# Optimization experiments

Measured on AMD Instinct MI355X. Metric: run time of the kernel, lower is better.

The kernel has to match this reference:

```python
import jax, jax.numpy as jnp
import numpy as np

B, HW, ENC, E, D, A, V, L = 64, 14, 2048, 512, 512, 512, 32000, 32
LN_EPS = 1e-5


def setup_inputs() -> dict:
    key = jax.random.key(0)
    ks = jax.random.split(key, 16)
    s = 0.02
    n = lambda k, sh: jax.random.normal(k, sh, jnp.float32)
    encoder_out = n(ks[0], (B, HW, HW, ENC))
    encoded_captions = jax.random.randint(ks[1], (B, L), 0, V)
    caption_lengths = jax.random.randint(ks[2], (B, 1), 2, L + 1)
    caption_lengths = caption_lengths.at[0, 0].set(L)  # ensure max length present
    return dict(
        encoder_out=encoder_out,
        encoded_captions=encoded_captions,
        caption_lengths=caption_lengths,
        emb=n(ks[3], (V, E)) * s,
        W_enc_att=n(ks[4], (A, ENC)) * s, b_enc_att=jnp.zeros((A,)),
        W_dec_att=n(ks[5], (A, D)) * s, b_dec_att=jnp.zeros((A,)),
        W_full_att=n(ks[6], (1, A)) * s, b_full_att=jnp.zeros((1,)),
        W_ih=n(ks[7], (4 * D, E + ENC)) * s, b_ih=jnp.zeros((4 * D,)),
        W_hh=n(ks[8], (4 * D, D)) * s, b_hh=jnp.zeros((4 * D,)),
        g_h=jnp.ones((D,)), be_h=jnp.zeros((D,)),
        g_c=jnp.ones((D,)), be_c=jnp.zeros((D,)),
        W_init_h=n(ks[9], (D, ENC)) * s, b_init_h=jnp.zeros((D,)),
        W_init_c=n(ks[10], (D, ENC)) * s, b_init_c=jnp.zeros((D,)),
        W_beta=n(ks[11], (ENC, D)) * s, b_beta=jnp.zeros((ENC,)),
        W_fc=n(ks[12], (V, D)) * s, b_fc=jnp.zeros((V,)),
    )


def _layer_norm(x, g, b):
    m = x.mean(-1, keepdims=True)
    v = ((x - m) ** 2).mean(-1, keepdims=True)
    return (x - m) / jnp.sqrt(v + LN_EPS) * g + b


def reference(encoder_out, encoded_captions, caption_lengths, emb,
              W_enc_att, b_enc_att, W_dec_att, b_dec_att, W_full_att, b_full_att,
              W_ih, b_ih, W_hh, b_hh, g_h, be_h, g_c, be_c,
              W_init_h, b_init_h, W_init_c, b_init_c, W_beta, b_beta, W_fc, b_fc):
    bsz = encoder_out.shape[0]
    enc_out = encoder_out.reshape(bsz, -1, encoder_out.shape[-1])  # [B,P,ENC]
    lengths = caption_lengths[:, 0]
    order = jnp.argsort(-lengths)  # stable descending sort (matches torch sort)
    lengths = lengths[order]
    enc_out = enc_out[order]
    caps = encoded_captions[order]
    embeds = emb[caps]  # [B,L,E]
    decode_lengths = lengths - 1
    T = caps.shape[1] - 1  # static max(decode_lengths)

    mean_enc = enc_out.mean(axis=1)
    h = _layer_norm(mean_enc @ W_init_h.T + b_init_h, g_h, be_h)
    c = _layer_norm(mean_enc @ W_init_c.T + b_init_c, g_c, be_c)

    att1 = enc_out @ W_enc_att.T + b_enc_att  # [B,P,A] precomputed once
    prev_seq = jnp.swapaxes(embeds[:, :T], 0, 1)  # [T,B,E] teacher-forced inputs
    masks = jnp.arange(T)[:, None] < decode_lengths[None, :]  # [T,B] active rows

    def step(carry, xs):
        h, c = carry
        prev, mask = xs
        # attention
        att2 = h @ W_dec_att.T + b_dec_att  # [B,A]
        e = jax.nn.relu(att1 + att2[:, None, :]) @ W_full_att[0] + b_full_att[0]  # [B,P]
        alpha = jax.nn.softmax(e, axis=1)
        awe = jnp.einsum('bpe,bp->be', enc_out, alpha)  # [B,ENC]
        gate = jax.nn.sigmoid(h @ W_beta.T + b_beta)
        awe = gate * awe
        # LSTM cell
        x = jnp.concatenate([prev, awe], axis=1)  # [B,E+ENC]
        gates = x @ W_ih.T + b_ih + h @ W_hh.T + b_hh
        i, f, g, o = jnp.split(gates, 4, axis=1)
        c_new = jax.nn.sigmoid(f) * c + jax.nn.sigmoid(i) * jnp.tanh(g)
        h_new = jax.nn.sigmoid(o) * jnp.tanh(c_new)
        h_new = _layer_norm(h_new, g_h, be_h)
        c_new = _layer_norm(c_new, g_c, be_c)
        preds = h_new @ W_fc.T + b_fc  # [B,V]; dropout is identity in eval
        m = mask[:, None]
        h = jnp.where(m, h_new, h)  # freeze finished rows (== torch batch shrink)
        c = jnp.where(m, c_new, c)
        return (h, c), (jnp.where(m, preds, 0.0), jnp.where(m, alpha, 0.0))

    (_, _), (preds_t, alphas_t) = jax.lax.scan(step, (h, c), (prev_seq, masks))
    predictions = jnp.swapaxes(preds_t, 0, 1)  # [B,T,V]
    alphas = jnp.swapaxes(alphas_t, 0, 1)      # [B,T,P]
    return predictions, caps, decode_lengths, alphas, order
```

## Files before the change

### kernel.cpp

```cpp
#include <hip/hip_runtime.h>
#include <cfloat>
#include <math.h>

#define B_ 64
#define P_ 196
#define ENC_ 2048
#define D_ 512
#define V_ 32000
#define L_ 32
#define T_ 31

#define OUT_PREDS 0L
#define OUT_CAPS  63488000L
#define OUT_DECL  63490048L
#define OUT_ALPH  63490112L
#define OUT_ORDER 63878976L

typedef __bf16 bf16;
typedef __bf16 bf16x8 __attribute__((ext_vector_type(8)));
typedef __bf16 bf16x4 __attribute__((ext_vector_type(4)));
typedef __bf16 bf16x2 __attribute__((ext_vector_type(2)));
typedef float  f32x4  __attribute__((ext_vector_type(4)));

static __device__ __forceinline__ float sigmoidf_(float x) { return 1.f / (1.f + __expf(-x)); }

__global__ void k_order(const int* __restrict__ cap_len, const int* __restrict__ caps,
                        int* __restrict__ order_i, int* __restrict__ declen_i,
                        int* __restrict__ caps_i, float* __restrict__ out)
{
    __shared__ int len_s[B_];
    int tid = threadIdx.x;
    len_s[tid] = cap_len[tid];
    __syncthreads();
    int li = len_s[tid];
    int pos = 0;
    for (int j = 0; j < B_; ++j) {
        int lj = len_s[j];
        pos += (lj > li) || (lj == li && j < tid);
    }
    order_i[pos]  = tid;
    declen_i[pos] = li - 1;
    out[OUT_ORDER + pos] = (float)tid;
    out[OUT_DECL  + pos] = (float)(li - 1);
    for (int l = 0; l < L_; ++l) {
        int tok = caps[tid * L_ + l];
        caps_i[pos * L_ + l] = tok;
        out[OUT_CAPS + pos * L_ + l] = (float)tok;
    }
}

__global__ __launch_bounds__(256) void k_cvt(const float* __restrict__ in, bf16* __restrict__ ob, long n)
{
    long i = ((long)blockIdx.x * 256 + threadIdx.x) * 8;
    if (i >= n) return;
    float4 a = *(const float4*)(in + i);
    float4 b = *(const float4*)(in + i + 4);
    bf16x8 v;
    v[0]=(bf16)a.x; v[1]=(bf16)a.y; v[2]=(bf16)a.z; v[3]=(bf16)a.w;
    v[4]=(bf16)b.x; v[5]=(bf16)b.y; v[6]=(bf16)b.z; v[7]=(bf16)b.w;
    *(bf16x8*)(ob + i) = v;
}

__global__ __launch_bounds__(256) void k_cvt_enc(const float* __restrict__ enc,
                                                 const int* __restrict__ order_i,
                                                 bf16* __restrict__ enc_s)
{
    long i = ((long)blockIdx.x * 256 + threadIdx.x) * 8;
    int b = (int)(i / ((long)P_ * ENC_));
    long rem = i - (long)b * P_ * ENC_;
    const float* src = enc + (long)order_i[b] * P_ * ENC_ + rem;
    float4 a = *(const float4*)(src);
    float4 c = *(const float4*)(src + 4);
    bf16x8 v;
    v[0]=(bf16)a.x; v[1]=(bf16)a.y; v[2]=(bf16)a.z; v[3]=(bf16)a.w;
    v[4]=(bf16)c.x; v[5]=(bf16)c.y; v[6]=(bf16)c.z; v[7]=(bf16)c.w;
    *(bf16x8*)(enc_s + i) = v;
}

__global__ __launch_bounds__(256) void k_meanb(const bf16* __restrict__ enc_s, bf16* __restrict__ mean_b)
{
    int b = blockIdx.x, col = blockIdx.y * 256 + threadIdx.x;
    float s = 0.f;
    const bf16* eb = enc_s + (long)b * P_ * ENC_ + col;
    for (int p = 0; p < P_; ++p) s += (float)eb[(long)p * ENC_];
    mean_b[(long)b * ENC_ + col] = (bf16)(s * (1.f / (float)P_));
}

template<int FUSE, int EPI, int SWZ>
__global__ void __launch_bounds__(256)
k_mgemm(const bf16* __restrict__ A, long lda,
        const bf16* __restrict__ B1, const bf16* __restrict__ B2,
        const float* __restrict__ bias,
        float* __restrict__ Cf, bf16* __restrict__ Cb,
        int N, int K, int kspl, int Nsp, int Ksp,
        const int* __restrict__ declen_i)
{
    const int tid = threadIdx.x;
    const int lane = tid & 63, w = tid >> 6;
    int mt, nt, z;
    if (SWZ == 0)      { mt = blockIdx.x; nt = blockIdx.y; z = blockIdx.z; }
    else if (SWZ == 1) { int o = blockIdx.x; int wg = (o & 7) * 98 + (o >> 3);
                         mt = wg >> 2; nt = wg & 3; z = 0; }
    else               { int o = blockIdx.x; int xcd = o & 7;
                         int base = xcd < 6 ? xcd * 969 : 5814 + (xcd - 6) * 968;
                         int wg = base + (o >> 3);
                         nt = wg / 31; mt = wg - 31 * nt; z = 0; }
    const int krange = K / kspl;
    const int k0 = z * krange, k1 = k0 + krange;
    const int r16 = lane & 15, kq = lane >> 4;
    const int koff = kq * 8;

    const bf16* Ap = A + (long)(mt * 64 + r16) * lda + koff;
    const int ncol0 = nt * 128 + w * 32;

    const bf16* Bp[2];
    const bf16* B2p[2];
#pragma unroll
    for (int ni = 0; ni < 2; ++ni) {
        int n = ncol0 + ni * 16 + r16;
        if (FUSE == 1)
            Bp[ni] = (n < Nsp) ? B1 + (long)n * K + koff
                               : B2 + (long)(n - Nsp) * K + koff;
        else if (FUSE == 2) {
            Bp[ni]  = B1 + (long)n * Ksp + koff;
            B2p[ni] = B2 + (long)n * (K - Ksp) + koff - Ksp;
        } else
            Bp[ni] = B1 + (long)n * K + koff;
    }

    auto loadA = [&](int kk, bf16x8* dst) {
#pragma unroll
        for (int mi = 0; mi < 4; ++mi)
            dst[mi] = *(const bf16x8*)(Ap + (long)mi * 16 * lda + kk);
    };
    auto loadB = [&](int kk, bf16x8* dst) {
#pragma unroll
        for (int ni = 0; ni < 2; ++ni) {
            if (FUSE == 2 && kk >= Ksp) dst[ni] = *(const bf16x8*)(B2p[ni] + kk);
            else                        dst[ni] = *(const bf16x8*)(Bp[ni] + kk);
        }
    };

    f32x4 acc[4][2] = {};
    bf16x8 af[4], bfr[2];
    loadA(k0, af); loadB(k0, bfr);
    for (int kk = k0 + 32; kk < k1; kk += 32) {
        bf16x8 af2[4], bf2[2];
        loadA(kk, af2); loadB(kk, bf2);
#pragma unroll
        for (int mi = 0; mi < 4; ++mi)
#pragma unroll
            for (int ni = 0; ni < 2; ++ni)
                acc[mi][ni] = __builtin_amdgcn_mfma_f32_16x16x32_bf16(bfr[ni], af[mi], acc[mi][ni], 0, 0, 0);
#pragma unroll
        for (int mi = 0; mi < 4; ++mi) af[mi] = af2[mi];
#pragma unroll
        for (int ni = 0; ni < 2; ++ni) bfr[ni] = bf2[ni];
    }
#pragma unroll
    for (int mi = 0; mi < 4; ++mi)
#pragma unroll
        for (int ni = 0; ni < 2; ++ni)
            acc[mi][ni] = __builtin_amdgcn_mfma_f32_16x16x32_bf16(bfr[ni], af[mi], acc[mi][ni], 0, 0, 0);

#pragma unroll
    for (int mi = 0; mi < 4; ++mi) {
        const int row = mt * 64 + mi * 16 + r16;
#pragma unroll
        for (int ni = 0; ni < 2; ++ni) {
            const int col = ncol0 + ni * 16 + kq * 4;
            f32x4 v = acc[mi][ni];
            if (EPI == 0) {
                *(f32x4*)(Cf + (long)z * 64 * N + (long)row * N + col) = v;
            } else if (EPI == 1) {
                f32x4 bv = *(const f32x4*)(bias + col);
                bf16x4 o;
                o[0]=(bf16)(v[0]+bv[0]); o[1]=(bf16)(v[1]+bv[1]);
                o[2]=(bf16)(v[2]+bv[2]); o[3]=(bf16)(v[3]+bv[3]);
                *(bf16x4*)(Cb + (long)row * N + col) = o;
            } else {
                int tt = row >> 6, b = row & 63;
                bool msk = tt < declen_i[b];
                f32x4 bv = *(const f32x4*)(bias + col);
                f32x4 o;
                o[0] = msk ? v[0]+bv[0] : 0.f; o[1] = msk ? v[1]+bv[1] : 0.f;
                o[2] = msk ? v[2]+bv[2] : 0.f; o[3] = msk ? v[3]+bv[3] : 0.f;
                *(f32x4*)(Cf + OUT_PREDS + ((long)b * T_ + tt) * V_ + col) = o;
            }
        }
    }
}

static __device__ __forceinline__ void ln_stats(float x, float* r1, float* r2,
                                                float& m, float& var)
{
    int tid = threadIdx.x;
    r1[tid] = x; r2[tid] = x * x;
    __syncthreads();
    for (int s = 256; s > 0; s >>= 1) {
        if (tid < s) { r1[tid] += r1[tid + s]; r2[tid] += r2[tid + s]; }
        __syncthreads();
    }
    m = r1[0] * (1.f / 512.f);
    var = r2[0] * (1.f / 512.f) - m * m;
    __syncthreads();
}

__global__ __launch_bounds__(512)
void k_initln(const float* __restrict__ pi,
              const float* __restrict__ b_h, const float* __restrict__ b_c,
              const float* __restrict__ g_h, const float* __restrict__ be_h,
              const float* __restrict__ g_c, const float* __restrict__ be_c,
              bf16* __restrict__ xh, float* __restrict__ c)
{
    int b = blockIdx.x, d = threadIdx.x;
    float yh = pi[(long)b * 1024 + d]       + b_h[d];
    float yc = pi[(long)b * 1024 + 512 + d] + b_c[d];
    __shared__ float r1[512], r2[512];
    float m, v;
    ln_stats(yh, r1, r2, m, v);
    xh[(long)b * 3072 + 2560 + d] = (bf16)((yh - m) * rsqrtf(v + 1e-5f) * g_h[d] + be_h[d]);
    ln_stats(yc, r1, r2, m, v);
    c[(long)b * 512 + d] = (yc - m) * rsqrtf(v + 1e-5f) * g_c[d] + be_c[d];
}

__global__ __launch_bounds__(256)
void k_alpha(const float* __restrict__ att2gate, const float* __restrict__ b_dec,
             const float* __restrict__ Wfull, const bf16* __restrict__ att1_b,
             const int* __restrict__ caps_i, const int* __restrict__ declen_i,
             const float* __restrict__ emb, float* __restrict__ alpha_b,
             bf16* __restrict__ xh, float* __restrict__ out, int t)
{
    const int b = blockIdx.x, tid = threadIdx.x;
    if (t >= declen_i[b]) {
        if (tid < P_) out[OUT_ALPH + ((long)b * T_ + t) * P_ + tid] = 0.f;
        return;
    }
    __shared__ float att2s[512], wf[512], red[256];
    for (int i = tid; i < 512; i += 256) {
        float s = b_dec[i];
#pragma unroll
        for (int zz = 0; zz < 4; ++zz) s += att2gate[((long)zz * 64 + b) * 2560 + i];
        att2s[i] = s;
        wf[i] = Wfull[i];
    }
    __syncthreads();
    float ev = -FLT_MAX;
    if (tid < P_) {
        const bf16* ar = att1_b + ((long)b * P_ + tid) * 512;
        float acc = 0.f;
        for (int a0 = 0; a0 < 512; a0 += 8) {
            bf16x8 v = *(const bf16x8*)(ar + a0);
#pragma unroll
            for (int j = 0; j < 8; ++j)
                acc += fmaxf((float)v[j] + att2s[a0 + j], 0.f) * wf[a0 + j];
        }
        ev = acc;
    }
    red[tid] = ev;
    __syncthreads();
    for (int s = 128; s > 0; s >>= 1) { if (tid < s) red[tid] = fmaxf(red[tid], red[tid + s]); __syncthreads(); }
    float mx = red[0];
    __syncthreads();
    float ex = (tid < P_) ? __expf(ev - mx) : 0.f;
    red[tid] = ex;
    __syncthreads();
    for (int s = 128; s > 0; s >>= 1) { if (tid < s) red[tid] += red[tid + s]; __syncthreads(); }
    float inv = 1.f / red[0];
    if (tid < P_) {
        float al = ex * inv;
        alpha_b[b * P_ + tid] = al;
        out[OUT_ALPH + ((long)b * T_ + t) * P_ + tid] = al;
    }
    int tok = caps_i[b * L_ + t];
    for (int i = tid; i < 512; i += 256)
        xh[(long)b * 3072 + i] = (bf16)emb[(long)tok * 512 + i];
}

__global__ __launch_bounds__(256)
void k_awe(const float* __restrict__ alpha_b, const float* __restrict__ att2gate,
           const float* __restrict__ b_beta, const bf16* __restrict__ enc_s,
           const int* __restrict__ declen_i, bf16* __restrict__ xh, int t)
{
    const int b = blockIdx.x, tid = threadIdx.x;
    if (t >= declen_i[b]) return;
    __shared__ float alp[P_];
    if (tid < P_) alp[tid] = alpha_b[b * P_ + tid];
    __syncthreads();
    const int col = blockIdx.y * 512 + tid * 2;
    const bf16* eb = enc_s + (long)b * P_ * ENC_ + col;
    float a0 = 0.f, a1 = 0.f;
#pragma unroll 4
    for (int p = 0; p < P_; ++p) {
        bf16x2 v = *(const bf16x2*)(eb + (long)p * ENC_);
        float al = alp[p];
        a0 += al * (float)v[0]; a1 += al * (float)v[1];
    }
    float g0 = b_beta[col], g1 = b_beta[col + 1];
#pragma unroll
    for (int zz = 0; zz < 4; ++zz) {
        const float* gs = att2gate + ((long)zz * 64 + b) * 2560 + 512 + col;
        g0 += gs[0]; g1 += gs[1];
    }
    bf16x2 o;
    o[0] = (bf16)(a0 * sigmoidf_(g0));
    o[1] = (bf16)(a1 * sigmoidf_(g1));
    *(bf16x2*)(xh + (long)b * 3072 + 512 + col) = o;
}

__global__ __launch_bounds__(512)
void k_lstm(const float* __restrict__ gp, const float* __restrict__ b_ih, const float* __restrict__ b_hh,
            const float* __restrict__ g_h, const float* __restrict__ be_h,
            const float* __restrict__ g_c, const float* __restrict__ be_c,
            bf16* __restrict__ xh, float* __restrict__ c, bf16* __restrict__ hseq,
            const int* __restrict__ declen_i, int t)
{
    int b = blockIdx.x, d = threadIdx.x;
    if (t >= declen_i[b]) return;
    float iv = b_ih[d]        + b_hh[d];
    float fv = b_ih[512 + d]  + b_hh[512 + d];
    float gv = b_ih[1024 + d] + b_hh[1024 + d];
    float ov = b_ih[1536 + d] + b_hh[1536 + d];
    for (int s = 0; s < 8; ++s) {
        const float* gs = gp + ((long)s * B_ + b) * 2048;
        iv += gs[d]; fv += gs[512 + d]; gv += gs[1024 + d]; ov += gs[1536 + d];
    }
    float cn = sigmoidf_(fv) * c[(long)b * 512 + d] + sigmoidf_(iv) * tanhf(gv);
    float hn = sigmoidf_(ov) * tanhf(cn);
    __shared__ float r1[512], r2[512];
    float m, v;
    ln_stats(hn, r1, r2, m, v);
    float hln = (hn - m) * rsqrtf(v + 1e-5f) * g_h[d] + be_h[d];
    ln_stats(cn, r1, r2, m, v);
    float cln = (cn - m) * rsqrtf(v + 1e-5f) * g_c[d] + be_c[d];
    bf16 hv = (bf16)hln;
    xh[(long)b * 3072 + 2560 + d] = hv;
    hseq[((long)t * B_ + b) * 512 + d] = hv;
    c[(long)b * 512 + d] = cln;
}

extern "C" void kernel_launch(void* const* d_in, const int* in_sizes, int n_in,
                              void* d_out, int out_size, void* d_ws, size_t ws_size,
                              hipStream_t stream)
{
    const float* enc       = (const float*)d_in[0];
    const int*   caps      = (const int*)  d_in[1];
    const int*   caplen    = (const int*)  d_in[2];
    const float* emb       = (const float*)d_in[3];
    const float* W_enc_att = (const float*)d_in[4];
    const float* b_enc_att = (const float*)d_in[5];
    const float* W_dec_att = (const float*)d_in[6];
    const float* b_dec_att = (const float*)d_in[7];
    const float* W_full    = (const float*)d_in[8];
    const float* W_ih      = (const float*)d_in[10];
    const float* b_ih      = (const float*)d_in[11];
    const float* W_hh      = (const float*)d_in[12];
    const float* b_hh      = (const float*)d_in[13];
    const float* g_h       = (const float*)d_in[14];
    const float* be_h      = (const float*)d_in[15];
    const float* g_c       = (const float*)d_in[16];
    const float* be_c      = (const float*)d_in[17];
    const float* W_init_h  = (const float*)d_in[18];
    const float* b_init_h  = (const float*)d_in[19];
    const float* W_init_c  = (const float*)d_in[20];
    const float* b_init_c  = (const float*)d_in[21];
    const float* W_beta    = (const float*)d_in[22];
    const float* b_beta    = (const float*)d_in[23];
    const float* W_fc      = (const float*)d_in[24];
    const float* b_fc      = (const float*)d_in[25];
    float* out = (float*)d_out;

    char* w = (char*)d_ws;
    auto alloc = [&](size_t bytes) { char* p = w; w += (bytes + 255) & ~(size_t)255; return p; };
    int*   order_i  = (int*)  alloc(B_ * 4);
    int*   declen_i = (int*)  alloc(B_ * 4);
    int*   caps_i   = (int*)  alloc(B_ * L_ * 4);
    bf16*  enc_s    = (bf16*) alloc((size_t)B_ * P_ * ENC_ * 2);
    bf16*  mean_b   = (bf16*) alloc((size_t)B_ * ENC_ * 2);
    bf16*  att1_b   = (bf16*) alloc((size_t)B_ * P_ * 512 * 2);
    float* pi       = (float*)alloc((size_t)B_ * 1024 * 4);
    float* att2gate = (float*)alloc((size_t)4 * B_ * 2560 * 4);
    float* alpha_b  = (float*)alloc((size_t)B_ * P_ * 4);
    bf16*  xh       = (bf16*) alloc((size_t)B_ * 3072 * 2);
    float* gp       = (float*)alloc((size_t)8 * B_ * 2048 * 4);
    float* cbuf     = (float*)alloc((size_t)B_ * 512 * 4);
    bf16*  hseq     = (bf16*) alloc((size_t)T_ * B_ * 512 * 2);
    bf16*  W_enc_b  = (bf16*) alloc((size_t)512 * 2048 * 2);
    bf16*  W_dec_b  = (bf16*) alloc((size_t)512 * 512 * 2);
    bf16*  W_beta_b = (bf16*) alloc((size_t)2048 * 512 * 2);
    bf16*  W_ih_b   = (bf16*) alloc((size_t)2048 * 2560 * 2);
    bf16*  W_hh_b   = (bf16*) alloc((size_t)2048 * 512 * 2);
    bf16*  W_fc_b   = (bf16*) alloc((size_t)32000 * 512 * 2);
    bf16*  W_inh_b  = (bf16*) alloc((size_t)512 * 2048 * 2);
    bf16*  W_inc_b  = (bf16*) alloc((size_t)512 * 2048 * 2);

    k_order<<<1, B_, 0, stream>>>(caplen, caps, order_i, declen_i, caps_i, out);
    k_cvt_enc<<<12544, 256, 0, stream>>>(enc, order_i, enc_s);
    k_meanb<<<dim3(B_, 8), 256, 0, stream>>>(enc_s, mean_b);

    auto cvt = [&](const float* src, bf16* dst, long n) {
        k_cvt<<<(int)((n / 8 + 255) / 256), 256, 0, stream>>>(src, dst, n);
    };
    cvt(W_enc_att, W_enc_b, 512L * 2048);
    cvt(W_dec_att, W_dec_b, 512L * 512);
    cvt(W_beta,    W_beta_b, 2048L * 512);
    cvt(W_ih,      W_ih_b,  2048L * 2560);
    cvt(W_hh,      W_hh_b,  2048L * 512);
    cvt(W_fc,      W_fc_b,  32000L * 512);
    cvt(W_init_h,  W_inh_b, 512L * 2048);
    cvt(W_init_c,  W_inc_b, 512L * 2048);

    k_mgemm<1, 0, 0><<<dim3(1, 8, 1), 256, 0, stream>>>(mean_b, 2048, W_inh_b, W_inc_b,
        nullptr, pi, nullptr, 1024, 2048, 1, 512, 0, nullptr);
    k_initln<<<B_, 512, 0, stream>>>(pi, b_init_h, b_init_c, g_h, be_h, g_c, be_c, xh, cbuf);

    k_mgemm<0, 1, 1><<<784, 256, 0, stream>>>(enc_s, 2048, W_enc_b, nullptr,
        b_enc_att, nullptr, att1_b, 512, 2048, 1, 0, 0, nullptr);

    for (int t = 0; t < T_; ++t) {
        k_mgemm<1, 0, 0><<<dim3(1, 20, 4), 256, 0, stream>>>(xh + 2560, 3072, W_dec_b, W_beta_b,
            nullptr, att2gate, nullptr, 2560, 512, 4, 512, 0, nullptr);
        k_alpha<<<B_, 256, 0, stream>>>(att2gate, b_dec_att, W_full, att1_b,
            caps_i, declen_i, emb, alpha_b, xh, out, t);
        k_awe<<<dim3(B_, 4), 256, 0, stream>>>(alpha_b, att2gate, b_beta, enc_s,
            declen_i, xh, t);
        k_mgemm<2, 0, 0><<<dim3(1, 16, 8), 256, 0, stream>>>(xh, 3072, W_ih_b, W_hh_b,
            nullptr, gp, nullptr, 2048, 3072, 8, 0, 2560, nullptr);
        k_lstm<<<B_, 512, 0, stream>>>(gp, b_ih, b_hh, g_h, be_h, g_c, be_c,
            xh, cbuf, hseq, declen_i, t);
    }

    k_mgemm<0, 2, 2><<<7750, 256, 0, stream>>>(hseq, 512, W_fc_b, nullptr,
        b_fc, out, nullptr, V_, 512, 1, 0, 0, declen_i);
}
```

Measured before the change: 2.516 ms.

## Fuse attention matvec into LSTM, merge alpha/awe, compact FC GEMM rows

```diff
diff --git a/kernel.cpp b/kernel.cpp
--- a/kernel.cpp
+++ b/kernel.cpp
@@ -26,9 +26,10 @@
 
 __global__ void k_order(const int* __restrict__ cap_len, const int* __restrict__ caps,
                         int* __restrict__ order_i, int* __restrict__ declen_i,
-                        int* __restrict__ caps_i, float* __restrict__ out)
-{
-    __shared__ int len_s[B_];
+                        int* __restrict__ caps_i, float* __restrict__ out,
+                        int* __restrict__ rmap, int* __restrict__ orow, int* __restrict__ mact)
+{
+    __shared__ int len_s[B_], dl_s[B_];
     int tid = threadIdx.x;
     len_s[tid] = cap_len[tid];
     __syncthreads();
@@ -40,12 +41,28 @@
     }
     order_i[pos]  = tid;
     declen_i[pos] = li - 1;
+    dl_s[pos]     = li - 1;
     out[OUT_ORDER + pos] = (float)tid;
     out[OUT_DECL  + pos] = (float)(li - 1);
     for (int l = 0; l < L_; ++l) {
         int tok = caps[tid * L_ + l];
         caps_i[pos * L_ + l] = tok;
         out[OUT_CAPS + pos * L_ + l] = (float)tok;
+    }
+    __syncthreads();
+    int p = tid;
+    int off = 0;
+    for (int j = 0; j < p; ++j) off += dl_s[j];
+    int dl = dl_s[p];
+    for (int tt = 0; tt < dl; ++tt) {
+        rmap[off + tt] = tt * B_ + p;
+        orow[off + tt] = p * T_ + tt;
+    }
+    if (p == B_ - 1) {
+        int M = off + dl;
+        mact[0] = M;
+        int Mr = (M + 63) & ~63;
+        for (int i = M; i < Mr; ++i) { rmap[i] = 0; orow[i] = -1; }
     }
 }
 
@@ -86,31 +103,26 @@
     mean_b[(long)b * ENC_ + col] = (bf16)(s * (1.f / (float)P_));
 }
 
-template<int FUSE, int EPI, int SWZ>
+template<int MI, int FUSE, int EPI, int SWZ>
 __global__ void __launch_bounds__(256)
 k_mgemm(const bf16* __restrict__ A, long lda,
         const bf16* __restrict__ B1, const bf16* __restrict__ B2,
         const float* __restrict__ bias,
         float* __restrict__ Cf, bf16* __restrict__ Cb,
-        int N, int K, int kspl, int Nsp, int Ksp,
-        const int* __restrict__ declen_i)
+        int N, int K, int kspl, int Nsp, int Ksp)
 {
     const int tid = threadIdx.x;
     const int lane = tid & 63, w = tid >> 6;
     int mt, nt, z;
-    if (SWZ == 0)      { mt = blockIdx.x; nt = blockIdx.y; z = blockIdx.z; }
-    else if (SWZ == 1) { int o = blockIdx.x; int wg = (o & 7) * 98 + (o >> 3);
-                         mt = wg >> 2; nt = wg & 3; z = 0; }
-    else               { int o = blockIdx.x; int xcd = o & 7;
-                         int base = xcd < 6 ? xcd * 969 : 5814 + (xcd - 6) * 968;
-                         int wg = base + (o >> 3);
-                         nt = wg / 31; mt = wg - 31 * nt; z = 0; }
+    if (SWZ == 0) { mt = blockIdx.x; nt = blockIdx.y; z = blockIdx.z; }
+    else          { int o = blockIdx.x; int wg = (o & 7) * 49 + (o >> 3);
+                    mt = wg >> 2; nt = wg & 3; z = 0; }
     const int krange = K / kspl;
     const int k0 = z * krange, k1 = k0 + krange;
     const int r16 = lane & 15, kq = lane >> 4;
     const int koff = kq * 8;
 
-    const bf16* Ap = A + (long)(mt * 64 + r16) * lda + koff;
+    const bf16* Ap = A + (long)(mt * (MI * 16) + r16) * lda + koff;
     const int ncol0 = nt * 128 + w * 32;
 
     const bf16* Bp[2];
@@ -130,7 +142,7 @@
 
     auto loadA = [&](int kk, bf16x8* dst) {
 #pragma unroll
-        for (int mi = 0; mi < 4; ++mi)
+        for (int mi = 0; mi < MI; ++mi)
             dst[mi] = *(const bf16x8*)(Ap + (long)mi * 16 * lda + kk);
     };
     auto loadB = [&](int kk, bf16x8* dst) {
@@ -141,51 +153,43 @@
         }
     };
 
-    f32x4 acc[4][2] = {};
-    bf16x8 af[4], bfr[2];
+    f32x4 acc[MI][2] = {};
+    bf16x8 af[MI], bfr[2];
     loadA(k0, af); loadB(k0, bfr);
     for (int kk = k0 + 32; kk < k1; kk += 32) {
-        bf16x8 af2[4], bf2[2];
+        bf16x8 af2[MI], bf2[2];
         loadA(kk, af2); loadB(kk, bf2);
 #pragma unroll
-        for (int mi = 0; mi < 4; ++mi)
+        for (int mi = 0; mi < MI; ++mi)
 #pragma unroll
             for (int ni = 0; ni < 2; ++ni)
                 acc[mi][ni] = __builtin_amdgcn_mfma_f32_16x16x32_bf16(bfr[ni], af[mi], acc[mi][ni], 0, 0, 0);
 #pragma unroll
-        for (int mi = 0; mi < 4; ++mi) af[mi] = af2[mi];
+        for (int mi = 0; mi < MI; ++mi) af[mi] = af2[mi];
 #pragma unroll
         for (int ni = 0; ni < 2; ++ni) bfr[ni] = bf2[ni];
     }
 #pragma unroll
-    for (int mi = 0; mi < 4; ++mi)
+    for (int mi = 0; mi < MI; ++mi)
 #pragma unroll
         for (int ni = 0; ni < 2; ++ni)
             acc[mi][ni] = __builtin_amdgcn_mfma_f32_16x16x32_bf16(bfr[ni], af[mi], acc[mi][ni], 0, 0, 0);
 
 #pragma unroll
-    for (int mi = 0; mi < 4; ++mi) {
-        const int row = mt * 64 + mi * 16 + r16;
+    for (int mi = 0; mi < MI; ++mi) {
+        const int row = mt * (MI * 16) + mi * 16 + r16;
 #pragma unroll
         for (int ni = 0; ni < 2; ++ni) {
             const int col = ncol0 + ni * 16 + kq * 4;
             f32x4 v = acc[mi][ni];
             if (EPI == 0) {
                 *(f32x4*)(Cf + (long)z * 64 * N + (long)row * N + col) = v;
-            } else if (EPI == 1) {
+            } else {
                 f32x4 bv = *(const f32x4*)(bias + col);
                 bf16x4 o;
                 o[0]=(bf16)(v[0]+bv[0]); o[1]=(bf16)(v[1]+bv[1]);
                 o[2]=(bf16)(v[2]+bv[2]); o[3]=(bf16)(v[3]+bv[3]);
                 *(bf16x4*)(Cb + (long)row * N + col) = o;
-            } else {
-                int tt = row >> 6, b = row & 63;
-                bool msk = tt < declen_i[b];
-                f32x4 bv = *(const f32x4*)(bias + col);
-                f32x4 o;
-                o[0] = msk ? v[0]+bv[0] : 0.f; o[1] = msk ? v[1]+bv[1] : 0.f;
-                o[2] = msk ? v[2]+bv[2] : 0.f; o[3] = msk ? v[3]+bv[3] : 0.f;
-                *(f32x4*)(Cf + OUT_PREDS + ((long)b * T_ + tt) * V_ + col) = o;
             }
         }
     }
@@ -204,6 +208,24 @@
     m = r1[0] * (1.f / 512.f);
     var = r2[0] * (1.f / 512.f) - m * m;
     __syncthreads();
+}
+
+static __device__ __forceinline__ void att2gate_mv(const float* h_s, const bf16* Wd,
+                                                   const bf16* Wbt, float* att2g, int b)
+{
+    const int d = threadIdx.x;
+#pragma unroll
+    for (int j = 0; j < 5; ++j) {
+        const int n = d + j * 512;
+        const bf16* wr = (n < 512) ? (Wd + (long)n * 512) : (Wbt + (long)(n - 512) * 512);
+        float acc = 0.f;
+        for (int k = 0; k < 512; k += 8) {
+            bf16x8 wv = *(const bf16x8*)(wr + k);
+#pragma unroll
+            for (int q = 0; q < 8; ++q) acc += h_s[k + q] * (float)wv[q];
+        }
+        att2g[(long)b * 2560 + n] = acc;
+    }
 }
 
 __global__ __launch_bounds__(512)
@@ -211,37 +233,40 @@
               const float* __restrict__ b_h, const float* __restrict__ b_c,
               const float* __restrict__ g_h, const float* __restrict__ be_h,
               const float* __restrict__ g_c, const float* __restrict__ be_c,
-              bf16* __restrict__ xh, float* __restrict__ c)
+              const bf16* __restrict__ Wd, const bf16* __restrict__ Wbt,
+              bf16* __restrict__ xh, float* __restrict__ c, float* __restrict__ att2g)
 {
     int b = blockIdx.x, d = threadIdx.x;
     float yh = pi[(long)b * 1024 + d]       + b_h[d];
     float yc = pi[(long)b * 1024 + 512 + d] + b_c[d];
-    __shared__ float r1[512], r2[512];
+    __shared__ float r1[512], r2[512], h_s[512];
     float m, v;
     ln_stats(yh, r1, r2, m, v);
-    xh[(long)b * 3072 + 2560 + d] = (bf16)((yh - m) * rsqrtf(v + 1e-5f) * g_h[d] + be_h[d]);
+    float hln = (yh - m) * rsqrtf(v + 1e-5f) * g_h[d] + be_h[d];
+    xh[(long)b * 3072 + 2560 + d] = (bf16)hln;
+    h_s[d] = hln;
     ln_stats(yc, r1, r2, m, v);
     c[(long)b * 512 + d] = (yc - m) * rsqrtf(v + 1e-5f) * g_c[d] + be_c[d];
+    __syncthreads();
+    att2gate_mv(h_s, Wd, Wbt, att2g, b);
 }
 
 __global__ __launch_bounds__(256)
-void k_alpha(const float* __restrict__ att2gate, const float* __restrict__ b_dec,
-             const float* __restrict__ Wfull, const bf16* __restrict__ att1_b,
-             const int* __restrict__ caps_i, const int* __restrict__ declen_i,
-             const float* __restrict__ emb, float* __restrict__ alpha_b,
-             bf16* __restrict__ xh, float* __restrict__ out, int t)
-{
-    const int b = blockIdx.x, tid = threadIdx.x;
+void k_attn(const float* __restrict__ att2g, const float* __restrict__ b_dec,
+            const float* __restrict__ b_beta, const float* __restrict__ Wfull,
+            const bf16* __restrict__ att1_b, const bf16* __restrict__ enc_s,
+            const int* __restrict__ caps_i, const int* __restrict__ declen_i,
+            const float* __restrict__ emb,
+            bf16* __restrict__ xh, float* __restrict__ out, int t)
+{
+    const int b = blockIdx.x >> 2, seg = blockIdx.x & 3, tid = threadIdx.x;
     if (t >= declen_i[b]) {
-        if (tid < P_) out[OUT_ALPH + ((long)b * T_ + t) * P_ + tid] = 0.f;
+        if (seg == 1 && tid < P_) out[OUT_ALPH + ((long)b * T_ + t) * P_ + tid] = 0.f;
         return;
     }
-    __shared__ float att2s[512], wf[512], red[256];
+    __shared__ float att2s[512], wf[512], red[256], alp[P_];
     for (int i = tid; i < 512; i += 256) {
-        float s = b_dec[i];
-#pragma unroll
-        for (int zz = 0; zz < 4; ++zz) s += att2gate[((long)zz * 64 + b) * 2560 + i];
-        att2s[i] = s;
+        att2s[i] = att2g[(long)b * 2560 + i] + b_dec[i];
         wf[i] = Wfull[i];
     }
     __syncthreads();
@@ -267,28 +292,12 @@
     __syncthreads();
     for (int s = 128; s > 0; s >>= 1) { if (tid < s) red[tid] += red[tid + s]; __syncthreads(); }
     float inv = 1.f / red[0];
-    if (tid < P_) {
-        float al = ex * inv;
-        alpha_b[b * P_ + tid] = al;
-        out[OUT_ALPH + ((long)b * T_ + t) * P_ + tid] = al;
-    }
-    int tok = caps_i[b * L_ + t];
-    for (int i = tid; i < 512; i += 256)
-        xh[(long)b * 3072 + i] = (bf16)emb[(long)tok * 512 + i];
-}
-
-__global__ __launch_bounds__(256)
-void k_awe(const float* __restrict__ alpha_b, const float* __restrict__ att2gate,
-           const float* __restrict__ b_beta, const bf16* __restrict__ enc_s,
-           const int* __restrict__ declen_i, bf16* __restrict__ xh, int t)
-{
-    const int b = blockIdx.x, tid = threadIdx.x;
-    if (t >= declen_i[b]) return;
-    __shared__ float alp[P_];
-    if (tid < P_) alp[tid] = alpha_b[b * P_ + tid];
-    __syncthreads();
-    const int col = blockIdx.y * 512 + tid * 2;
-    const bf16* eb = enc_s + (long)b * P_ * ENC_ + col;
+    if (tid < P_) alp[tid] = ex * inv;
+    __syncthreads();
+    if (seg == 1 && tid < P_)
+        out[OUT_ALPH + ((long)b * T_ + t) * P_ + tid] = alp[tid];
+    const int c0 = seg * 512 + tid * 2;
+    const bf16* eb = enc_s + (long)b * P_ * ENC_ + c0;
     float a0 = 0.f, a1 = 0.f;
 #pragma unroll 4
     for (int p = 0; p < P_; ++p) {
@@ -296,24 +305,26 @@
         float al = alp[p];
         a0 += al * (float)v[0]; a1 += al * (float)v[1];
     }
-    float g0 = b_beta[col], g1 = b_beta[col + 1];
-#pragma unroll
-    for (int zz = 0; zz < 4; ++zz) {
-        const float* gs = att2gate + ((long)zz * 64 + b) * 2560 + 512 + col;
-        g0 += gs[0]; g1 += gs[1];
-    }
+    float g0 = b_beta[c0]     + att2g[(long)b * 2560 + 512 + c0];
+    float g1 = b_beta[c0 + 1] + att2g[(long)b * 2560 + 512 + c0 + 1];
     bf16x2 o;
     o[0] = (bf16)(a0 * sigmoidf_(g0));
     o[1] = (bf16)(a1 * sigmoidf_(g1));
-    *(bf16x2*)(xh + (long)b * 3072 + 512 + col) = o;
+    *(bf16x2*)(xh + (long)b * 3072 + 512 + c0) = o;
+    if (seg == 0) {
+        int tok = caps_i[b * L_ + t];
+        for (int i = tid; i < 512; i += 256)
+            xh[(long)b * 3072 + i] = (bf16)emb[(long)tok * 512 + i];
+    }
 }
 
 __global__ __launch_bounds__(512)
 void k_lstm(const float* __restrict__ gp, const float* __restrict__ b_ih, const float* __restrict__ b_hh,
             const float* __restrict__ g_h, const float* __restrict__ be_h,
             const float* __restrict__ g_c, const float* __restrict__ be_c,
+            const bf16* __restrict__ Wd, const bf16* __restrict__ Wbt,
             bf16* __restrict__ xh, float* __restrict__ c, bf16* __restrict__ hseq,
-            const int* __restrict__ declen_i, int t)
+            float* __restrict__ att2g, const int* __restrict__ declen_i, int t)
 {
     int b = blockIdx.x, d = threadIdx.x;
     if (t >= declen_i[b]) return;
@@ -321,13 +332,14 @@
     float fv = b_ih[512 + d]  + b_hh[512 + d];
     float gv = b_ih[1024 + d] + b_hh[1024 + d];
     float ov = b_ih[1536 + d] + b_hh[1536 + d];
+#pragma unroll
     for (int s = 0; s < 8; ++s) {
         const float* gs = gp + ((long)s * B_ + b) * 2048;
         iv += gs[d]; fv += gs[512 + d]; gv += gs[1024 + d]; ov += gs[1536 + d];
     }
     float cn = sigmoidf_(fv) * c[(long)b * 512 + d] + sigmoidf_(iv) * tanhf(gv);
     float hn = sigmoidf_(ov) * tanhf(cn);
-    __shared__ float r1[512], r2[512];
+    __shared__ float r1[512], r2[512], h_s[512];
     float m, v;
     ln_stats(hn, r1, r2, m, v);
     float hln = (hn - m) * rsqrtf(v + 1e-5f) * g_h[d] + be_h[d];
@@ -337,6 +349,98 @@
     xh[(long)b * 3072 + 2560 + d] = hv;
     hseq[((long)t * B_ + b) * 512 + d] = hv;
     c[(long)b * 512 + d] = cln;
+    h_s[d] = hln;
+    __syncthreads();
+    att2gate_mv(h_s, Wd, Wbt, att2g, b);
+}
+
+__global__ __launch_bounds__(256) void k_zero(const int* __restrict__ declen_i, float* __restrict__ out)
+{
+    int x = blockIdx.x;
+    int b = x / T_, t = x - b * T_;
+    if (t < declen_i[b]) return;
+    float4 z = {0.f, 0.f, 0.f, 0.f};
+    long base = OUT_PREDS + ((long)b * T_ + t) * V_;
+    for (int i = threadIdx.x * 4; i < V_; i += 1024)
+        *(float4*)(out + base + i) = z;
+}
+
+__global__ __launch_bounds__(256)
+void k_preds(const bf16* __restrict__ hseq, const bf16* __restrict__ Wfc,
+             const float* __restrict__ bias,
+             const int* __restrict__ rmap, const int* __restrict__ orow,
+             const int* __restrict__ mact, float* __restrict__ out)
+{
+    int o = blockIdx.x; int xcd = o & 7;
+    int base = xcd < 6 ? xcd * 969 : 5814 + (xcd - 6) * 968;
+    int wg = base + (o >> 3);
+    int nt = wg / 31, mt = wg - 31 * nt;
+    if (mt * 64 >= mact[0]) return;
+    __shared__ int rs[64], os[64];
+    __shared__ __align__(16) float ct[64][132];
+    const int tid = threadIdx.x, lane = tid & 63, w = tid >> 6;
+    const int r16 = lane & 15, kq = lane >> 4, koff = kq * 8;
+    if (tid < 64) { rs[tid] = rmap[mt * 64 + tid]; os[tid] = orow[mt * 64 + tid]; }
+    __syncthreads();
+    const int ncol0 = nt * 128 + w * 32;
+    const bf16* Ap[4];
+#pragma unroll
+    for (int mi = 0; mi < 4; ++mi)
+        Ap[mi] = hseq + (long)rs[mi * 16 + r16] * 512 + koff;
+    const bf16* Bp[2];
+#pragma unroll
+    for (int ni = 0; ni < 2; ++ni)
+        Bp[ni] = Wfc + (long)(ncol0 + ni * 16 + r16) * 512 + koff;
+
+    f32x4 acc[4][2] = {};
+    bf16x8 af[4], bfr[2];
+#pragma unroll
+    for (int mi = 0; mi < 4; ++mi) af[mi] = *(const bf16x8*)(Ap[mi]);
+#pragma unroll
+    for (int ni = 0; ni < 2; ++ni) bfr[ni] = *(const bf16x8*)(Bp[ni]);
+    for (int kk = 32; kk < 512; kk += 32) {
+        bf16x8 af2[4], bf2[2];
+#pragma unroll
+        for (int mi = 0; mi < 4; ++mi) af2[mi] = *(const bf16x8*)(Ap[mi] + kk);
+#pragma unroll
+        for (int ni = 0; ni < 2; ++ni) bf2[ni] = *(const bf16x8*)(Bp[ni] + kk);
+#pragma unroll
+        for (int mi = 0; mi < 4; ++mi)
+#pragma unroll
+            for (int ni = 0; ni < 2; ++ni)
+                acc[mi][ni] = __builtin_amdgcn_mfma_f32_16x16x32_bf16(bfr[ni], af[mi], acc[mi][ni], 0, 0, 0);
+#pragma unroll
+        for (int mi = 0; mi < 4; ++mi) af[mi] = af2[mi];
+#pragma unroll
+        for (int ni = 0; ni < 2; ++ni) bfr[ni] = bf2[ni];
+    }
+#pragma unroll
+    for (int mi = 0; mi < 4; ++mi)
+#pragma unroll
+        for (int ni = 0; ni < 2; ++ni)
+            acc[mi][ni] = __builtin_amdgcn_mfma_f32_16x16x32_bf16(bfr[ni], af[mi], acc[mi][ni], 0, 0, 0);
+
+#pragma unroll
+    for (int mi = 0; mi < 4; ++mi)
+#pragma unroll
+        for (int ni = 0; ni < 2; ++ni)
+            *(f32x4*)&ct[mi * 16 + r16][w * 32 + ni * 16 + kq * 4] = acc[mi][ni];
+    __syncthreads();
+    const int r0 = tid >> 5, cc = (tid & 31) * 4;
+    const int gcol = nt * 128 + cc;
+    f32x4 bv = *(const f32x4*)(bias + gcol);
+#pragma unroll
+    for (int it = 0; it < 8; ++it) {
+        int r = it * 8 + r0;
+        int orv = os[r];
+        if (orv >= 0) {
+            f32x4 v = *(f32x4*)&ct[r][cc];
+            f32x4 oo;
+            oo[0] = v[0] + bv[0]; oo[1] = v[1] + bv[1];
+            oo[2] = v[2] + bv[2]; oo[3] = v[3] + bv[3];
+            *(f32x4*)(out + OUT_PREDS + (long)orv * V_ + gcol) = oo;
+        }
+    }
 }
 
 extern "C" void kernel_launch(void* const* d_in, const int* in_sizes, int n_in,
@@ -375,12 +479,14 @@
     int*   order_i  = (int*)  alloc(B_ * 4);
     int*   declen_i = (int*)  alloc(B_ * 4);
     int*   caps_i   = (int*)  alloc(B_ * L_ * 4);
+    int*   rmap     = (int*)  alloc(2048 * 4);
+    int*   orow     = (int*)  alloc(2048 * 4);
+    int*   mact     = (int*)  alloc(256);
     bf16*  enc_s    = (bf16*) alloc((size_t)B_ * P_ * ENC_ * 2);
     bf16*  mean_b   = (bf16*) alloc((size_t)B_ * ENC_ * 2);
     bf16*  att1_b   = (bf16*) alloc((size_t)B_ * P_ * 512 * 2);
     float* pi       = (float*)alloc((size_t)B_ * 1024 * 4);
-    float* att2gate = (float*)alloc((size_t)4 * B_ * 2560 * 4);
-    float* alpha_b  = (float*)alloc((size_t)B_ * P_ * 4);
+    float* att2g    = (float*)alloc((size_t)B_ * 2560 * 4);
     bf16*  xh       = (bf16*) alloc((size_t)B_ * 3072 * 2);
     float* gp       = (float*)alloc((size_t)8 * B_ * 2048 * 4);
     float* cbuf     = (float*)alloc((size_t)B_ * 512 * 4);
@@ -394,7 +500,7 @@
     bf16*  W_inh_b  = (bf16*) alloc((size_t)512 * 2048 * 2);
     bf16*  W_inc_b  = (bf16*) alloc((size_t)512 * 2048 * 2);
 
-    k_order<<<1, B_, 0, stream>>>(caplen, caps, order_i, declen_i, caps_i, out);
+    k_order<<<1, B_, 0, stream>>>(caplen, caps, order_i, declen_i, caps_i, out, rmap, orow, mact);
     k_cvt_enc<<<12544, 256, 0, stream>>>(enc, order_i, enc_s);
     k_meanb<<<dim3(B_, 8), 256, 0, stream>>>(enc_s, mean_b);
 
@@ -410,26 +516,23 @@
     cvt(W_init_h,  W_inh_b, 512L * 2048);
     cvt(W_init_c,  W_inc_b, 512L * 2048);
 
-    k_mgemm<1, 0, 0><<<dim3(1, 8, 1), 256, 0, stream>>>(mean_b, 2048, W_inh_b, W_inc_b,
-        nullptr, pi, nullptr, 1024, 2048, 1, 512, 0, nullptr);
-    k_initln<<<B_, 512, 0, stream>>>(pi, b_init_h, b_init_c, g_h, be_h, g_c, be_c, xh, cbuf);
-
-    k_mgemm<0, 1, 1><<<784, 256, 0, stream>>>(enc_s, 2048, W_enc_b, nullptr,
-        b_enc_att, nullptr, att1_b, 512, 2048, 1, 0, 0, nullptr);
+    k_mgemm<4, 1, 0, 0><<<dim3(1, 8, 1), 256, 0, stream>>>(mean_b, 2048, W_inh_b, W_inc_b,
+        nullptr, pi, nullptr, 1024, 2048, 1, 512, 0);
+    k_initln<<<B_, 512, 0, stream>>>(pi, b_init_h, b_init_c, g_h, be_h, g_c, be_c,
+        W_dec_b, W_beta_b, xh, cbuf, att2g);
+
+    k_mgemm<8, 0, 1, 1><<<392, 256, 0, stream>>>(enc_s, 2048, W_enc_b, nullptr,
+        b_enc_att, nullptr, att1_b, 512, 2048, 1, 0, 0);
 
     for (int t = 0; t < T_; ++t) {
-        k_mgemm<1, 0, 0><<<dim3(1, 20, 4), 256, 0, stream>>>(xh + 2560, 3072, W_dec_b, W_beta_b,
-            nullptr, att2gate, nullptr, 2560, 512, 4, 512, 0, nullptr);
-        k_alpha<<<B_, 256, 0, stream>>>(att2gate, b_dec_att, W_full, att1_b,
-            caps_i, declen_i, emb, alpha_b, xh, out, t);
-        k_awe<<<dim3(B_, 4), 256, 0, stream>>>(alpha_b, att2gate, b_beta, enc_s,
-            declen_i, xh, t);
-        k_mgemm<2, 0, 0><<<dim3(1, 16, 8), 256, 0, stream>>>(xh, 3072, W_ih_b, W_hh_b,
-            nullptr, gp, nullptr, 2048, 3072, 8, 0, 2560, nullptr);
+        k_attn<<<256, 256, 0, stream>>>(att2g, b_dec_att, b_beta, W_full, att1_b, enc_s,
+            caps_i, declen_i, emb, xh, out, t);
+        k_mgemm<4, 2, 0, 0><<<dim3(1, 16, 8), 256, 0, stream>>>(xh, 3072, W_ih_b, W_hh_b,
+            nullptr, gp, nullptr, 2048, 3072, 8, 0, 2560);
         k_lstm<<<B_, 512, 0, stream>>>(gp, b_ih, b_hh, g_h, be_h, g_c, be_c,
-            xh, cbuf, hseq, declen_i, t);
-    }
-
-    k_mgemm<0, 2, 2><<<7750, 256, 0, stream>>>(hseq, 512, W_fc_b, nullptr,
-        b_fc, out, nullptr, V_, 512, 1, 0, 0, declen_i);
-}
+            W_dec_b, W_beta_b, xh, cbuf, hseq, att2g, declen_i, t);
+    }
+
+    k_zero<<<B_ * T_, 256, 0, stream>>>(declen_i, out);
+    k_preds<<<7750, 256, 0, stream>>>(hseq, W_fc_b, b_fc, rmap, orow, mact, out);
+}
```

New measurement: 4.495 ms. 1.79x slower.
